# Optimization experiments

Measured on AMD Instinct MI355X. Metric: run time of the kernel, lower is better.

## Reference

```python
import jax, jax.numpy as jnp
import numpy as np

I_T = 0.5       # IoU threshold self.I_t
GAMMA = 2.0     # focal loss gamma
EPS = 1e-7      # focal loss eps clamp
BS, P, C_IN = 8, 2048, 512


def pairwise_iou(b):
    # b: (bs, P, 4) xyxy -> (bs, P, P), same math as torchvision box_iou (no +1)
    area = (b[..., 2] - b[..., 0]) * (b[..., 3] - b[..., 1])
    lt = jnp.maximum(b[:, :, None, :2], b[:, None, :, :2])
    rb = jnp.minimum(b[:, :, None, 2:], b[:, None, :, 2:])
    wh = jnp.clip(rb - lt, 0.0, None)
    inter = wh[..., 0] * wh[..., 1]
    return inter / (area[:, :, None] + area[:, None, :] - inter)


def assign_labels_weights(pre_score, labels, rois):
    # Vectorized, order-faithful version of the per-batch/per-class python loop.
    # Selected seeds per class c: proposals with pre_score[...,c] > 0.5 if more than
    # one, else the single argmax proposal (torch code falls back when k<=1).
    # Sequential `_I > old` running max over (c, j) in ascending order is equivalent
    # to a global first-occurrence argmax (strict >), so per-class max + running
    # compare with earlier-class tie preference reproduces it exactly.
    bs, Pn = pre_score.shape[0], pre_score.shape[1]
    iou = pairwise_iou(rois)                      # (bs, P, P)
    run_I = jnp.full((bs, Pn), -1.0, pre_score.dtype)
    run_w = jnp.ones((bs, Pn), pre_score.dtype)
    hits = []
    for c in range(3):
        s = pre_score[:, :, c]                    # (bs, P)
        th = s > 0.5
        cnt = th.sum(-1)
        onehot = jnp.arange(Pn)[None, :] == jnp.argmax(s, -1)[:, None]
        sel = jnp.where((cnt > 1)[:, None], th, onehot)
        sel = sel & (labels[:, c] != 0)[:, None]  # skip classes absent from image
        masked = jnp.where(sel[:, None, :], iou, -2.0)  # (bs, P, P)
        val = masked.max(-1)                      # best IoU vs any seed of class c
        jidx = masked.argmax(-1)
        cand_x = jnp.take_along_axis(s, jidx, axis=1)
        better = val > run_I
        run_w = jnp.where(better, cand_x, run_w)
        run_I = jnp.where(better, val, run_I)
        hits.append(val > I_T)
    hit = jnp.stack(hits, -1)                     # (bs, P, 3)
    bg = (~hit.any(-1))[..., None]
    y = jnp.concatenate([hit.astype(pre_score.dtype), bg.astype(pre_score.dtype)], -1)
    return y, run_w


def icr_forward(inputs, fc_w, fc_b, pre_score, labels, rois, num):
    bs = inputs.shape[0] // num
    xr = inputs @ fc_w + fc_b                     # (bs*P, 4)
    logit = jax.nn.softmax(xr.reshape(bs, num, 4), -1)
    ps = jax.lax.stop_gradient(pre_score)         # .clone().detach()
    lb = jax.lax.stop_gradient(labels)
    y, w = assign_labels_weights(ps, lb, rois)
    y = y.reshape(bs * num, 4)
    w = w.reshape(bs * num, 1)
    # FocalLoss(gamma=2, mode='none')
    p = jnp.clip(jax.nn.softmax(xr, -1), EPS, 1.0 - EPS)
    fl = -y * jnp.log(p) * (1.0 - p) ** GAMMA
    imbalance = y.sum(0)                          # (4,)
    loss = (w * fl / (imbalance + 1e-7)).reshape(bs, num, 4)
    lab = lb.at[:, 3].set(1.0)[:, None, :]        # lab[:,0,3]=1
    w_ = 10.0 * jnp.exp(logit) * (1.0 - lab) + lab
    loss = (loss * w_).sum() / bs
    return logit, loss


def setup_inputs():
    key = jax.random.key(0)
    k = jax.random.split(key, 6)
    inputs = jax.random.normal(k[0], (BS * P, C_IN), jnp.float32)
    fc_w = jax.random.normal(k[1], (C_IN, 4), jnp.float32) * 0.02
    fc_b = jnp.zeros((4,), jnp.float32)
    pre_score = jax.random.uniform(k[2], (BS, P, 4), dtype=jnp.float32)
    labels = (jax.random.uniform(k[3], (BS, 4)) < 0.5).astype(jnp.float32)
    labels = labels.at[:, 3].set(0.0)
    xy = jax.random.uniform(k[4], (BS, P, 2), dtype=jnp.float32) * 448.0
    wh = jax.random.uniform(k[5], (BS, P, 2), dtype=jnp.float32) * 63.0 + 1.0
    rois = jnp.concatenate([xy, xy + wh], -1)     # valid xyxy boxes in 512x512
    return {"inputs": inputs, "fc_w": fc_w, "fc_b": fc_b, "pre_score": pre_score,
            "labels": labels, "rois": rois, "num": P}


def reference(inputs, fc_w, fc_b, pre_score, labels, rois, num):
    return icr_forward(inputs, fc_w, fc_b, pre_score, labels, rois, num)
```

## Files before the change

### kernel.cpp

```cpp
#include <hip/hip_runtime.h>

#define BSZ 8
#define PN  2048
#define CIN 512
#define CAP 2048
#define NW  16


__global__ __launch_bounds__(256) void k_front(
    const float* __restrict__ inp, const float* __restrict__ fcw,
    const float* __restrict__ fcb, const float* __restrict__ ps,
    const float* __restrict__ labels, const float* __restrict__ rois,
    float* __restrict__ logit, float* __restrict__ accum,
    int* __restrict__ meta, float* __restrict__ sList,
    float* __restrict__ areaL, float4* __restrict__ roiList)
{
  const int t = threadIdx.x;
  if (blockIdx.x >= 24) {
    const int gw   = (((int)blockIdx.x - 24) * 256 + t) >> 6;
    const int lane = t & 63;
    const int kb   = lane << 2;
    const float4 wa0 = *(const float4*)(fcw + (kb + 0) * 4);
    const float4 wa1 = *(const float4*)(fcw + (kb + 1) * 4);
    const float4 wa2 = *(const float4*)(fcw + (kb + 2) * 4);
    const float4 wa3 = *(const float4*)(fcw + (kb + 3) * 4);
    const float4 wb0 = *(const float4*)(fcw + (256 + kb + 0) * 4);
    const float4 wb1 = *(const float4*)(fcw + (256 + kb + 1) * 4);
    const float4 wb2 = *(const float4*)(fcw + (256 + kb + 2) * 4);
    const float4 wb3 = *(const float4*)(fcw + (256 + kb + 3) * 4);
    const float4 bias = *(const float4*)fcb;
    #pragma unroll
    for (int rr = 0; rr < 4; ++rr) {
      const int r = (gw << 2) + rr;
      const float* row = inp + r * CIN;
      const float4 xa = *(const float4*)(row + kb);
      const float4 xb = *(const float4*)(row + 256 + kb);
      float a0 = xa.x*wa0.x + xa.y*wa1.x + xa.z*wa2.x + xa.w*wa3.x
               + xb.x*wb0.x + xb.y*wb1.x + xb.z*wb2.x + xb.w*wb3.x;
      float a1 = xa.x*wa0.y + xa.y*wa1.y + xa.z*wa2.y + xa.w*wa3.y
               + xb.x*wb0.y + xb.y*wb1.y + xb.z*wb2.y + xb.w*wb3.y;
      float a2 = xa.x*wa0.z + xa.y*wa1.z + xa.z*wa2.z + xa.w*wa3.z
               + xb.x*wb0.z + xb.y*wb1.z + xb.z*wb2.z + xb.w*wb3.z;
      float a3 = xa.x*wa0.w + xa.y*wa1.w + xa.z*wa2.w + xa.w*wa3.w
               + xb.x*wb0.w + xb.y*wb1.w + xb.z*wb2.w + xb.w*wb3.w;
      #pragma unroll
      for (int off = 32; off; off >>= 1) {
        a0 += __shfl_xor(a0, off); a1 += __shfl_xor(a1, off);
        a2 += __shfl_xor(a2, off); a3 += __shfl_xor(a3, off);
      }
      if (lane == 0) {
        a0 += bias.x; a1 += bias.y; a2 += bias.z; a3 += bias.w;
        const float m  = fmaxf(fmaxf(a0, a1), fmaxf(a2, a3));
        const float e0 = expf(a0 - m), e1 = expf(a1 - m);
        const float e2 = expf(a2 - m), e3 = expf(a3 - m);
        const float inv = 1.0f / (e0 + e1 + e2 + e3);
        float4 o; o.x = e0*inv; o.y = e1*inv; o.z = e2*inv; o.w = e3*inv;
        *(float4*)(logit + r * 4) = o;
      }
    }
    return;
  }

  const int bc = blockIdx.x;
  if (bc == 0 && t < 12) accum[t] = 0.0f;
  const int b = bc / 3;
  const int c = bc % 3;
  const int j0 = t * 8;

  float sv[8];
  int   flg = 0, cnt = 0;
  float vmax = -1e30f;
  int   jmax = 0;
  #pragma unroll
  for (int m = 0; m < 8; ++m) {
    const float s = ps[(b * PN + j0 + m) * 4 + c];
    sv[m] = s;
    if (s > 0.5f) { flg |= 1 << m; ++cnt; }
    if (s > vmax) { vmax = s; jmax = j0 + m; }
  }

  __shared__ float lv[256];
  __shared__ int   lj[256];
  __shared__ int   pre[256];
  lv[t] = vmax; lj[t] = jmax; pre[t] = cnt;
  __syncthreads();
  for (int off = 128; off > 0; off >>= 1) {
    if (t < off) {
      const float v2 = lv[t + off]; const int j2 = lj[t + off];
      if (v2 > lv[t] || (v2 == lv[t] && j2 < lj[t])) { lv[t] = v2; lj[t] = j2; }
    }
    __syncthreads();
  }
  for (int off = 1; off < 256; off <<= 1) {
    const int add = (t >= off) ? pre[t - off] : 0;
    __syncthreads();
    pre[t] += add;
    __syncthreads();
  }
  const int  totalTh = pre[255];
  const int  excl    = pre[t] - cnt;
  const int  jArg    = lj[0];
  const bool lab     = labels[b * 4 + c] != 0.0f;
  const int  L    = (!lab) ? 0 : ((totalTh > 1) ? totalTh : 1);
  const int  Lpad = (L + 7) & ~7;

  __shared__ float4 lastRoi;
  __shared__ float  lastS, lastA;
  float4* dstR = roiList + bc * CAP;
  float*  dstS = sList   + bc * CAP;
  float*  dstA = areaL   + bc * CAP;
  const float4* rb = ((const float4*)rois) + b * PN;

  if (lab) {
    if (totalTh > 1) {
      int pos = excl;
      #pragma unroll
      for (int m = 0; m < 8; ++m) {
        if (flg & (1 << m)) {
          const float4 r = rb[j0 + m];
          const float  a = (r.z - r.x) * (r.w - r.y);
          dstR[pos] = r; dstS[pos] = sv[m]; dstA[pos] = a;
          if (pos == L - 1) { lastRoi = r; lastS = sv[m]; lastA = a; }
          ++pos;
        }
      }
    } else if (t == (jArg >> 3)) {
      const float4 r = rb[jArg];
      const float  a = (r.z - r.x) * (r.w - r.y);
      dstR[0] = r; dstS[0] = sv[jArg & 7]; dstA[0] = a;
      lastRoi = r; lastS = sv[jArg & 7]; lastA = a;
    }
  }
  __syncthreads();
  if (t < Lpad - L) { dstR[L + t] = lastRoi; dstS[L + t] = lastS; dstA[L + t] = lastA; }
  if (t == 0) meta[bc] = Lpad;
}

__global__ __launch_bounds__(1024, 8) void k_assign(
    const float* __restrict__ rois, const int* __restrict__ meta,
    const float4* __restrict__ roiList, const float* __restrict__ areaL,
    float* __restrict__ pbn, float* __restrict__ pbd, int* __restrict__ pbp)
{
  const int blk   = blockIdx.x;
  const int h     = blk & 1;
  const int itile = (blk >> 1) & 31;
  const int b     = blk >> 6;
  const int t     = threadIdx.x;
  const int lane  = t & 63;
  const int wv    = t >> 6;

  __shared__ __align__(16) char ldsraw[61440];
  float4* sroi  = (float4*)ldsraw;
  float*  sarea = (float*)(ldsraw + 49152);
  float*  mn    = (float*)ldsraw;
  float*  md    = (float*)(ldsraw + 12288);
  int*    mp    = (int*)(ldsraw + 24576);

  int startc[3], cntc[3];
  #pragma unroll
  for (int c = 0; c < 3; ++c) {
    const int L  = meta[b * 3 + c];
    const int L2 = ((L >> 1) + 7) & ~7;
    const int s0 = h ? L2 : 0;
    const int e0 = h ? L  : L2;
    startc[c] = s0;
    cntc[c]   = e0 - s0;
    if (t < cntc[c]) {
      sroi [c * 1024 + t] = roiList[(b * 3 + c) * CAP + s0 + t];
      sarea[c * 1024 + t] = areaL  [(b * 3 + c) * CAP + s0 + t];
    }
  }
  const int i = (itile << 6) + lane;
  const float4 ri = ((const float4*)rois)[b * PN + i];
  const float areai = (ri.z - ri.x) * (ri.w - ri.y);
  __syncthreads();

  float BN[3], BD[3]; int BP[3];
  #pragma unroll
  for (int c = 0; c < 3; ++c) {
    const int cnt = cntc[c];
    const int C   = (((cnt + 15) >> 4) + 7) & ~7;
    const int g0  = wv * C;
    int g1 = g0 + C; if (g1 > cnt) g1 = cnt;
    float nA = -2.0f, dA = 1.0f, nB = -2.0f, dB = 1.0f;
    int   pA = 0, pB = 0;
    const float4* rbase = sroi  + c * 1024;
    const float*  abase = sarea + c * 1024;

    auto upd = [&](float& n, float& d, int& p,
                   const float4 rj, const float aj, const int pos) {
      const float lx = fmaxf(ri.x, rj.x), ly = fmaxf(ri.y, rj.y);
      const float rx = fminf(ri.z, rj.z), ry = fminf(ri.w, rj.w);
      const float ww = fmaxf(rx - lx, 0.0f), hh = fmaxf(ry - ly, 0.0f);
      const float inter = ww * hh;
      const float uni   = areai + aj - inter;
      if (inter * d > n * uni) { n = inter; d = uni; p = pos; }
    };

    for (int g = g0; g < g1; g += 4) {
      const float4 r0 = rbase[g], r1 = rbase[g+1], r2 = rbase[g+2], r3 = rbase[g+3];
      const float  a0 = abase[g], a1 = abase[g+1], a2 = abase[g+2], a3 = abase[g+3];
      upd(nA, dA, pA, r0, a0, g);
      upd(nB, dB, pB, r2, a2, g + 2);
      upd(nA, dA, pA, r1, a1, g + 1);
      upd(nB, dB, pB, r3, a3, g + 3);
    }
    const float tB = nB * dA, tA = nA * dB;
    if (tB > tA || (tB == tA && pB < pA)) { nA = nB; dA = dB; pA = pB; }
    BN[c] = nA; BD[c] = dA; BP[c] = pA + startc[c];
  }
  __syncthreads();
  #pragma unroll
  for (int c = 0; c < 3; ++c) {
    mn[(c * NW + wv) * 64 + lane] = BN[c];
    md[(c * NW + wv) * 64 + lane] = BD[c];
    mp[(c * NW + wv) * 64 + lane] = BP[c];
  }
  __syncthreads();
  if (wv == 0) {
    #pragma unroll
    for (int c = 0; c < 3; ++c) {
      float bn = BN[c], bd = BD[c]; int bp = BP[c];
      for (int w2 = 1; w2 < NW; ++w2) {
        const float n = mn[(c * NW + w2) * 64 + lane];
        const float d = md[(c * NW + w2) * 64 + lane];
        const int   p = mp[(c * NW + w2) * 64 + lane];
        if (n * bd > bn * d) { bn = n; bd = d; bp = p; }
      }
      const int o = ((b * 3 + c) * 2 + h) * PN + i;
      pbn[o] = bn; pbd[o] = bd; pbp[o] = bp;
    }
  }
}

__global__ __launch_bounds__(256) void k_back(
    const float* __restrict__ pbn, const float* __restrict__ pbd,
    const int* __restrict__ pbp, const float* __restrict__ sList,
    const float* __restrict__ logit, const float* __restrict__ labels,
    float* __restrict__ accum, float* __restrict__ loss)
{
  const int t  = threadIdx.x;
  const int gi = blockIdx.x * 256 + t;
  const int b  = gi >> 11;
  const int i  = gi & (PN - 1);

  float v[3], sc[3];
  #pragma unroll
  for (int c = 0; c < 3; ++c) {
    const int o0 = ((b * 3 + c) * 2) * PN + i;
    float n = pbn[o0], d = pbd[o0]; int p = pbp[o0];
    const float n1 = pbn[o0 + PN], d1 = pbd[o0 + PN];
    const int   p1 = pbp[o0 + PN];
    if (n1 * d > n * d1) { n = n1; d = d1; p = p1; }
    v[c]  = n / d;
    sc[c] = sList[(b * 3 + c) * CAP + p];
  }
  float runI = -1.0f, runw = 1.0f;
  if (v[0] > runI) { runw = sc[0]; runI = v[0]; }
  if (v[1] > runI) { runw = sc[1]; runI = v[1]; }
  if (v[2] > runI) { runw = sc[2]; runI = v[2]; }
  const float y0 = (v[0] > 0.5f) ? 1.0f : 0.0f;
  const float y1 = (v[1] > 0.5f) ? 1.0f : 0.0f;
  const float y2 = (v[2] > 0.5f) ? 1.0f : 0.0f;
  const float y3 = (y0 + y1 + y2 == 0.0f) ? 1.0f : 0.0f;

  const float4 lg = ((const float4*)logit)[gi];
  const float lb0 = labels[b * 4 + 0];
  const float lb1 = labels[b * 4 + 1];
  const float lb2 = labels[b * 4 + 2];

  auto term = [&](const float l, const float yv, const float labv) -> float {
    const float p  = fminf(fmaxf(l, 1e-7f), 1.0f - 1e-7f);
    const float om = 1.0f - p;
    const float fl = -yv * logf(p) * om * om;
    const float wl = 10.0f * expf(l) * (1.0f - labv) + labv;
    return runw * fl * wl;
  };
  float s[8];
  s[0] = term(lg.x, y0, lb0); s[1] = term(lg.y, y1, lb1);
  s[2] = term(lg.z, y2, lb2); s[3] = term(lg.w, y3, 1.0f);
  s[4] = y0; s[5] = y1; s[6] = y2; s[7] = y3;

  #pragma unroll
  for (int k = 0; k < 8; ++k)
    #pragma unroll
    for (int off = 32; off; off >>= 1) s[k] += __shfl_xor(s[k], off);

  __shared__ float red[4][8];
  const int wv = t >> 6;
  if ((t & 63) == 0)
    #pragma unroll
    for (int k = 0; k < 8; ++k) red[wv][k] = s[k];
  __syncthreads();
  if (t < 8) {
    const float sum = red[0][t] + red[1][t] + red[2][t] + red[3][t];
    atomicAdd(&accum[t], sum);
  }
  __syncthreads();
  if (t == 0) {
    __threadfence();
    const int ticket = __hip_atomic_fetch_add((int*)(accum + 8), 1,
                        __ATOMIC_ACQ_REL, __HIP_MEMORY_SCOPE_AGENT);
    if (ticket == 63) {
      float L = 0.0f;
      #pragma unroll
      for (int c = 0; c < 4; ++c) {
        const float num = __hip_atomic_load(accum + c,
                            __ATOMIC_RELAXED, __HIP_MEMORY_SCOPE_AGENT);
        const float den = __hip_atomic_load(accum + 4 + c,
                            __ATOMIC_RELAXED, __HIP_MEMORY_SCOPE_AGENT);
        L += num / (den + 1e-7f);
      }
      loss[0] = L * 0.125f;
    }
  }
}

extern "C" void kernel_launch(void* const* d_in, const int* in_sizes, int n_in,
                              void* d_out, int out_size, void* d_ws, size_t ws_size,
                              hipStream_t stream)
{
  (void)in_sizes; (void)n_in; (void)out_size; (void)ws_size;
  const float* inp    = (const float*)d_in[0];
  const float* fcw    = (const float*)d_in[1];
  const float* fcb    = (const float*)d_in[2];
  const float* ps     = (const float*)d_in[3];
  const float* labels = (const float*)d_in[4];
  const float* rois   = (const float*)d_in[5];
  float* out = (float*)d_out;

  char* ws = (char*)d_ws;
  float*  accum   = (float*) (ws);
  int*    meta    = (int*)   (ws + 64);
  float*  sList   = (float*) (ws + 1024);
  float*  areaL   = (float*) (ws + 197632);
  float4* roiL    = (float4*)(ws + 394240);
  float*  pbn     = (float*) (ws + 1180672);
  float*  pbd     = (float*) (ws + 1573888);
  int*    pbp     = (int*)   (ws + 1967104);

  k_front <<<1048, 256, 0, stream>>>(inp, fcw, fcb, ps, labels, rois,
                                     out, accum, meta, sList, areaL, roiL);
  k_assign<<<512, 1024, 0, stream>>>(rois, meta, roiL, areaL, pbn, pbd, pbp);
  k_back  <<<64,   256, 0, stream>>>(pbn, pbd, pbp, sList, out, labels, accum,
                                     out + BSZ * PN * 4);
}
```

Baseline: 116.5 us.

## Fuse assign and loss kernels, stream seeds per class, recompute seed areas

Merges the back-end loss kernel into the IoU assignment kernel, so the partial best-IoU buffers and a third launch go away. Each block now covers a full class seed list, loading it class by class into shared memory instead of splitting the list across two blocks. Seed areas are recomputed in the inner loop rather than stored and loaded. In exchange there are half as many blocks (256) doing twice the work each, with extra barriers per class and a small amount of added arithmetic per pair.

```diff
diff --git a/kernel.cpp b/kernel.cpp
--- a/kernel.cpp
+++ b/kernel.cpp
@@ -13,7 +13,7 @@
     const float* __restrict__ labels, const float* __restrict__ rois,
     float* __restrict__ logit, float* __restrict__ accum,
     int* __restrict__ meta, float* __restrict__ sList,
-    float* __restrict__ areaL, float4* __restrict__ roiList)
+    float4* __restrict__ roiList)
 {
   const int t = threadIdx.x;
   if (blockIdx.x >= 24) {
@@ -105,10 +105,9 @@
   const int  Lpad = (L + 7) & ~7;
 
   __shared__ float4 lastRoi;
-  __shared__ float  lastS, lastA;
+  __shared__ float  lastS;
   float4* dstR = roiList + bc * CAP;
   float*  dstS = sList   + bc * CAP;
-  float*  dstA = areaL   + bc * CAP;
   const float4* rb = ((const float4*)rois) + b * PN;
 
   if (lab) {
@@ -118,142 +117,103 @@
       for (int m = 0; m < 8; ++m) {
         if (flg & (1 << m)) {
           const float4 r = rb[j0 + m];
-          const float  a = (r.z - r.x) * (r.w - r.y);
-          dstR[pos] = r; dstS[pos] = sv[m]; dstA[pos] = a;
-          if (pos == L - 1) { lastRoi = r; lastS = sv[m]; lastA = a; }
+          dstR[pos] = r; dstS[pos] = sv[m];
+          if (pos == L - 1) { lastRoi = r; lastS = sv[m]; }
           ++pos;
         }
       }
     } else if (t == (jArg >> 3)) {
       const float4 r = rb[jArg];
-      const float  a = (r.z - r.x) * (r.w - r.y);
-      dstR[0] = r; dstS[0] = sv[jArg & 7]; dstA[0] = a;
-      lastRoi = r; lastS = sv[jArg & 7]; lastA = a;
+      dstR[0] = r; dstS[0] = sv[jArg & 7];
+      lastRoi = r; lastS = sv[jArg & 7];
     }
   }
   __syncthreads();
-  if (t < Lpad - L) { dstR[L + t] = lastRoi; dstS[L + t] = lastS; dstA[L + t] = lastA; }
+  if (t < Lpad - L) { dstR[L + t] = lastRoi; dstS[L + t] = lastS; }
   if (t == 0) meta[bc] = Lpad;
 }
 
-__global__ __launch_bounds__(1024, 8) void k_assign(
+__global__ __launch_bounds__(1024, 4) void k_assign(
     const float* __restrict__ rois, const int* __restrict__ meta,
-    const float4* __restrict__ roiList, const float* __restrict__ areaL,
-    float* __restrict__ pbn, float* __restrict__ pbd, int* __restrict__ pbp)
+    const float4* __restrict__ roiList, const float* __restrict__ sList,
+    const float* __restrict__ logit, const float* __restrict__ labels,
+    float* __restrict__ accum, float* __restrict__ loss)
 {
-  const int blk   = blockIdx.x;
-  const int h     = blk & 1;
-  const int itile = (blk >> 1) & 31;
-  const int b     = blk >> 6;
-  const int t     = threadIdx.x;
-  const int lane  = t & 63;
-  const int wv    = t >> 6;
-
-  __shared__ __align__(16) char ldsraw[61440];
-  float4* sroi  = (float4*)ldsraw;
-  float*  sarea = (float*)(ldsraw + 49152);
-  float*  mn    = (float*)ldsraw;
-  float*  md    = (float*)(ldsraw + 12288);
-  int*    mp    = (int*)(ldsraw + 24576);
-
-  int startc[3], cntc[3];
-  #pragma unroll
-  for (int c = 0; c < 3; ++c) {
-    const int L  = meta[b * 3 + c];
-    const int L2 = ((L >> 1) + 7) & ~7;
-    const int s0 = h ? L2 : 0;
-    const int e0 = h ? L  : L2;
-    startc[c] = s0;
-    cntc[c]   = e0 - s0;
-    if (t < cntc[c]) {
-      sroi [c * 1024 + t] = roiList[(b * 3 + c) * CAP + s0 + t];
-      sarea[c * 1024 + t] = areaL  [(b * 3 + c) * CAP + s0 + t];
-    }
-  }
-  const int i = (itile << 6) + lane;
+  const int blk  = blockIdx.x;
+  const int t    = threadIdx.x;
+  const int lane = t & 63;
+  const int wv   = t >> 6;
+  const int b    = blk >> 5;
+  const int it   = blk & 31;
+
+  __shared__ __align__(16) float4 sroi[2048];
+  __shared__ float smn[NW][64];
+  __shared__ float smd[NW][64];
+  __shared__ int   smp[NW][64];
+
+  const int i = (it << 6) + lane;
   const float4 ri = ((const float4*)rois)[b * PN + i];
   const float areai = (ri.z - ri.x) * (ri.w - ri.y);
-  __syncthreads();
-
-  float BN[3], BD[3]; int BP[3];
-  #pragma unroll
+
+  auto upd = [&](float& n, float& d, int& p, const float4 rj, const int pos) {
+    const float aj = (rj.z - rj.x) * (rj.w - rj.y);
+    const float lx = fmaxf(ri.x, rj.x), ly = fmaxf(ri.y, rj.y);
+    const float rx = fminf(ri.z, rj.z), ry = fminf(ri.w, rj.w);
+    const float ww = fmaxf(rx - lx, 0.0f), hh = fmaxf(ry - ly, 0.0f);
+    const float inter = ww * hh;
+    const float uni   = areai + aj - inter;
+    if (inter * d > n * uni) { n = inter; d = uni; p = pos; }
+  };
+
+  float BNf[3], BDf[3]; int BPf[3];
+
   for (int c = 0; c < 3; ++c) {
-    const int cnt = cntc[c];
-    const int C   = (((cnt + 15) >> 4) + 7) & ~7;
-    const int g0  = wv * C;
+    const int cnt = meta[b * 3 + c];
+    const float4* src = roiList + (b * 3 + c) * CAP;
+    if (t < cnt)        sroi[t]        = src[t];
+    if (t + 1024 < cnt) sroi[t + 1024] = src[t + 1024];
+    __syncthreads();
+
+    const int C  = (((cnt + 15) >> 4) + 7) & ~7;
+    const int g0 = wv * C;
     int g1 = g0 + C; if (g1 > cnt) g1 = cnt;
     float nA = -2.0f, dA = 1.0f, nB = -2.0f, dB = 1.0f;
     int   pA = 0, pB = 0;
-    const float4* rbase = sroi  + c * 1024;
-    const float*  abase = sarea + c * 1024;
-
-    auto upd = [&](float& n, float& d, int& p,
-                   const float4 rj, const float aj, const int pos) {
-      const float lx = fmaxf(ri.x, rj.x), ly = fmaxf(ri.y, rj.y);
-      const float rx = fminf(ri.z, rj.z), ry = fminf(ri.w, rj.w);
-      const float ww = fmaxf(rx - lx, 0.0f), hh = fmaxf(ry - ly, 0.0f);
-      const float inter = ww * hh;
-      const float uni   = areai + aj - inter;
-      if (inter * d > n * uni) { n = inter; d = uni; p = pos; }
-    };
-
     for (int g = g0; g < g1; g += 4) {
-      const float4 r0 = rbase[g], r1 = rbase[g+1], r2 = rbase[g+2], r3 = rbase[g+3];
-      const float  a0 = abase[g], a1 = abase[g+1], a2 = abase[g+2], a3 = abase[g+3];
-      upd(nA, dA, pA, r0, a0, g);
-      upd(nB, dB, pB, r2, a2, g + 2);
-      upd(nA, dA, pA, r1, a1, g + 1);
-      upd(nB, dB, pB, r3, a3, g + 3);
+      const float4 r0 = sroi[g],     r1 = sroi[g + 1];
+      const float4 r2 = sroi[g + 2], r3 = sroi[g + 3];
+      upd(nA, dA, pA, r0, g);
+      upd(nB, dB, pB, r2, g + 2);
+      upd(nA, dA, pA, r1, g + 1);
+      upd(nB, dB, pB, r3, g + 3);
     }
     const float tB = nB * dA, tA = nA * dB;
     if (tB > tA || (tB == tA && pB < pA)) { nA = nB; dA = dB; pA = pB; }
-    BN[c] = nA; BD[c] = dA; BP[c] = pA + startc[c];
-  }
-  __syncthreads();
-  #pragma unroll
-  for (int c = 0; c < 3; ++c) {
-    mn[(c * NW + wv) * 64 + lane] = BN[c];
-    md[(c * NW + wv) * 64 + lane] = BD[c];
-    mp[(c * NW + wv) * 64 + lane] = BP[c];
-  }
-  __syncthreads();
-  if (wv == 0) {
-    #pragma unroll
-    for (int c = 0; c < 3; ++c) {
-      float bn = BN[c], bd = BD[c]; int bp = BP[c];
+
+    smn[wv][lane] = nA; smd[wv][lane] = dA; smp[wv][lane] = pA;
+    __syncthreads();
+    if (wv == 0) {
+      float bn = nA, bd = dA; int bp = pA;
+      #pragma unroll 1
       for (int w2 = 1; w2 < NW; ++w2) {
-        const float n = mn[(c * NW + w2) * 64 + lane];
-        const float d = md[(c * NW + w2) * 64 + lane];
-        const int   p = mp[(c * NW + w2) * 64 + lane];
+        const float n = smn[w2][lane];
+        const float d = smd[w2][lane];
+        const int   p = smp[w2][lane];
         if (n * bd > bn * d) { bn = n; bd = d; bp = p; }
       }
-      const int o = ((b * 3 + c) * 2 + h) * PN + i;
-      pbn[o] = bn; pbd[o] = bd; pbp[o] = bp;
-    }
-  }
-}
-
-__global__ __launch_bounds__(256) void k_back(
-    const float* __restrict__ pbn, const float* __restrict__ pbd,
-    const int* __restrict__ pbp, const float* __restrict__ sList,
-    const float* __restrict__ logit, const float* __restrict__ labels,
-    float* __restrict__ accum, float* __restrict__ loss)
-{
-  const int t  = threadIdx.x;
-  const int gi = blockIdx.x * 256 + t;
-  const int b  = gi >> 11;
-  const int i  = gi & (PN - 1);
-
+      BNf[c] = bn; BDf[c] = bd; BPf[c] = bp;
+    }
+    __syncthreads();
+  }
+
+  if (wv != 0) return;
+
+  const int gi = b * PN + i;
   float v[3], sc[3];
   #pragma unroll
   for (int c = 0; c < 3; ++c) {
-    const int o0 = ((b * 3 + c) * 2) * PN + i;
-    float n = pbn[o0], d = pbd[o0]; int p = pbp[o0];
-    const float n1 = pbn[o0 + PN], d1 = pbd[o0 + PN];
-    const int   p1 = pbp[o0 + PN];
-    if (n1 * d > n * d1) { n = n1; d = d1; p = p1; }
-    v[c]  = n / d;
-    sc[c] = sList[(b * 3 + c) * CAP + p];
+    v[c]  = BNf[c] / BDf[c];
+    sc[c] = sList[(b * 3 + c) * CAP + BPf[c]];
   }
   float runI = -1.0f, runw = 1.0f;
   if (v[0] > runI) { runw = sc[0]; runI = v[0]; }
@@ -286,22 +246,13 @@
     #pragma unroll
     for (int off = 32; off; off >>= 1) s[k] += __shfl_xor(s[k], off);
 
-  __shared__ float red[4][8];
-  const int wv = t >> 6;
-  if ((t & 63) == 0)
+  if (lane == 0) {
     #pragma unroll
-    for (int k = 0; k < 8; ++k) red[wv][k] = s[k];
-  __syncthreads();
-  if (t < 8) {
-    const float sum = red[0][t] + red[1][t] + red[2][t] + red[3][t];
-    atomicAdd(&accum[t], sum);
-  }
-  __syncthreads();
-  if (t == 0) {
+    for (int k = 0; k < 8; ++k) atomicAdd(&accum[k], s[k]);
     __threadfence();
     const int ticket = __hip_atomic_fetch_add((int*)(accum + 8), 1,
                         __ATOMIC_ACQ_REL, __HIP_MEMORY_SCOPE_AGENT);
-    if (ticket == 63) {
+    if (ticket == 255) {
       float L = 0.0f;
       #pragma unroll
       for (int c = 0; c < 4; ++c) {
@@ -333,15 +284,10 @@
   float*  accum   = (float*) (ws);
   int*    meta    = (int*)   (ws + 64);
   float*  sList   = (float*) (ws + 1024);
-  float*  areaL   = (float*) (ws + 197632);
   float4* roiL    = (float4*)(ws + 394240);
-  float*  pbn     = (float*) (ws + 1180672);
-  float*  pbd     = (float*) (ws + 1573888);
-  int*    pbp     = (int*)   (ws + 1967104);
-
-  k_front <<<1048, 256, 0, stream>>>(inp, fcw, fcb, ps, labels, rois,
-                                     out, accum, meta, sList, areaL, roiL);
-  k_assign<<<512, 1024, 0, stream>>>(rois, meta, roiL, areaL, pbn, pbd, pbp);
-  k_back  <<<64,   256, 0, stream>>>(pbn, pbd, pbp, sList, out, labels, accum,
-                                     out + BSZ * PN * 4);
+
+  k_front <<<1048, 256,  0, stream>>>(inp, fcw, fcb, ps, labels, rois,
+                                      out, accum, meta, sList, roiL);
+  k_assign<<<256,  1024, 0, stream>>>(rois, meta, roiL, sList, out, labels,
+                                      accum, out + BSZ * PN * 4);
 }
```

Result: slower. 136.7 us (+17.4%).
